# Kernel optimization log

Measured on AMD Instinct MI355X. Metric: run time of the kernel, lower is better.

The kernel has to match this reference:

```python
import jax, jax.numpy as jnp
import numpy as np

K = 20
EPS = 1e-5
NEG_SLOPE = 0.2


def knn(x, k):
    # x: [B, C, N] -> idx [B, N, k] of nearest neighbors (negative sq-dist topk)
    inner = -2.0 * jnp.einsum('bcn,bcm->bnm', x, x)
    xx = jnp.sum(x * x, axis=1)  # [B, N]
    d = -xx[:, :, None] - inner - xx[:, None, :]
    return jax.lax.top_k(d, k)[1]


def get_graph_feature(x, k):
    # x: [B, C, N] -> [B, 2C, N, k]
    idx = knn(x, k)
    xt = jnp.transpose(x, (0, 2, 1))            # [B, N, C]
    feat = jax.vmap(lambda a, i: a[i])(xt, idx)  # [B, N, k, C]
    center = xt[:, :, None, :]
    out = jnp.concatenate([feat - center, jnp.broadcast_to(center, feat.shape)], axis=-1)
    return jnp.transpose(out, (0, 3, 1, 2))


def conv_bn_lrelu(x, w, g, b):
    # 1x1 conv + BatchNorm2d (batch stats, training mode) + LeakyReLU(0.2)
    y = jnp.einsum('oc,bcnk->bonk', w, x)
    mu = jnp.mean(y, axis=(0, 2, 3), keepdims=True)
    var = jnp.mean((y - mu) ** 2, axis=(0, 2, 3), keepdims=True)
    y = (y - mu) * jax.lax.rsqrt(var + EPS)
    y = y * g[None, :, None, None] + b[None, :, None, None]
    return jnp.where(y >= 0, y, NEG_SLOPE * y)


def lrelu(y):
    return jnp.where(y >= 0, y, NEG_SLOPE * y)


def setup_inputs() -> dict:
    key = jax.random.key(0)
    ks = jax.random.split(key, 24)
    B, N = 8, 4096
    d = {}
    d['x'] = jax.random.normal(ks[0], (B, 3, N), dtype=jnp.float32)
    def wconv(k_, o, c):
        return jax.random.normal(k_, (o, c), dtype=jnp.float32) * (1.0 / np.sqrt(c))
    d['w1'] = wconv(ks[1], 32, 6)
    d['g1'] = 1.0 + 0.1 * jax.random.normal(ks[2], (32,), dtype=jnp.float32)
    d['b1'] = 0.1 * jax.random.normal(ks[3], (32,), dtype=jnp.float32)
    d['w2'] = wconv(ks[4], 64, 70)
    d['g2'] = 1.0 + 0.1 * jax.random.normal(ks[5], (64,), dtype=jnp.float32)
    d['b2'] = 0.1 * jax.random.normal(ks[6], (64,), dtype=jnp.float32)
    d['wd1'] = wconv(ks[7], 64, 64)
    d['gd1'] = 1.0 + 0.1 * jax.random.normal(ks[8], (64,), dtype=jnp.float32)
    d['bd1'] = 0.1 * jax.random.normal(ks[9], (64,), dtype=jnp.float32)
    d['wd2'] = wconv(ks[10], 64, 128)
    d['gd2'] = 1.0 + 0.1 * jax.random.normal(ks[11], (64,), dtype=jnp.float32)
    d['bd2'] = 0.1 * jax.random.normal(ks[12], (64,), dtype=jnp.float32)
    d['W2d'] = jax.random.normal(ks[13], (128, 128), dtype=jnp.float32) * (1.0 / np.sqrt(128))
    d['b2d'] = 0.1 * jax.random.normal(ks[14], (128,), dtype=jnp.float32)
    d['W3d'] = jax.random.normal(ks[15], (64, 128), dtype=jnp.float32) * (1.0 / np.sqrt(128))
    d['b3d'] = 0.1 * jax.random.normal(ks[16], (64,), dtype=jnp.float32)
    d['W4d'] = jax.random.normal(ks[17], (11, 64), dtype=jnp.float32) * (1.0 / np.sqrt(64))
    d['b4d'] = 0.1 * jax.random.normal(ks[18], (11,), dtype=jnp.float32)
    return d


def reference(x, w1, g1, b1, w2, g2, b2, wd1, gd1, bd1, wd2, gd2, bd2,
              W2d, b2d, W3d, b3d, W4d, b4d):
    x1_gf = get_graph_feature(x, K)                    # [B, 6, N, k]
    x1_max = jnp.max(conv_bn_lrelu(x1_gf, w1, g1, b1), axis=-1)  # [B, 32, N]
    x2_gf = jnp.concatenate([x1_gf, get_graph_feature(x1_max, K)], axis=1)  # [B, 70, N, k]
    x2_max = jnp.max(conv_bn_lrelu(x2_gf, w2, g2, b2), axis=-1)  # [B, 64, N]
    xd1 = jnp.max(conv_bn_lrelu(get_graph_feature(x1_max, K), wd1, gd1, bd1), axis=-1)  # [B, 64, N]
    xd2 = jnp.max(conv_bn_lrelu(get_graph_feature(x2_max, K), wd2, gd2, bd2), axis=-1)  # [B, 64, N]
    h = jnp.concatenate([xd1, xd2], axis=1)            # [B, 128, N]
    h = h.reshape(1, -1, 128)                          # faithful row-major view
    h = jnp.mean(h, axis=1)                            # [1, 128]
    h = lrelu(h @ W2d.T + b2d)
    h = lrelu(h @ W3d.T + b3d)
    return lrelu(h @ W4d.T + b4d)                      # [1, 11]
```

## Files before the change

### kernel.cpp

```cpp
#include <hip/hip_runtime.h>

#define BB 8
#define NN 4096
#define KK 20
constexpr float EPSV = 1e-5f;
constexpr float SLOPE = 0.2f;

typedef __bf16 bfrag __attribute__((ext_vector_type(8)));
typedef float floatx4 __attribute__((ext_vector_type(4)));
typedef unsigned short us8 __attribute__((ext_vector_type(8)));

__device__ __forceinline__ float lrelu(float v) { return v >= 0.f ? v : SLOPE * v; }

__device__ __forceinline__ unsigned short bf16rn(float f) {
    unsigned int u = __float_as_uint(f);
    return (unsigned short)((u + 0x7FFFu + ((u >> 16) & 1u)) >> 16);
}
__device__ __forceinline__ float bf16up(unsigned short h) {
    return __uint_as_float(((unsigned int)h) << 16);
}

__device__ __forceinline__ void gl2lds16(const void* g, void* l) {
    __builtin_amdgcn_global_load_lds(
        (const __attribute__((address_space(1))) unsigned int*)g,
        (__attribute__((address_space(3))) unsigned int*)l, 16, 0, 0);
}

__global__ void zero_kernel(float* p, int n) {
    int i = blockIdx.x * 256 + threadIdx.x;
    if (i < n) p[i] = 0.f;
}

template<int C>
__global__ void halfnorm_kernel(const float* __restrict__ src, float* __restrict__ hng) {
    int n = blockIdx.x * 256 + threadIdx.x;
    int b = blockIdx.y;
    float s = 0.f;
    #pragma unroll
    for (int c = 0; c < C; c++) { float v = src[(b * C + c) * NN + n]; s += v * v; }
    hng[b * NN + n] = 0.5f * s;
}

template<int C>
__global__ void pack_kernel(const float* __restrict__ src, unsigned short* __restrict__ pk) {
    constexpr int NCH = C / 4;
    int i = blockIdx.x * 256 + threadIdx.x;
    int b = blockIdx.y;
    int n = i / NCH, j = i % NCH;
    us8 v;
    if (j < C / 8) {
        int c0 = j * 8;
        #pragma unroll
        for (int cc = 0; cc < 8; cc++)
            v[cc] = bf16rn(src[(b * C + c0 + cc) * NN + n]);
    } else {
        int c0 = (j - C / 8) * 8;
        #pragma unroll
        for (int cc = 0; cc < 8; cc++) {
            float f = src[(b * C + c0 + cc) * NN + n];
            unsigned short h = bf16rn(f);
            v[cc] = bf16rn(f - bf16up(h));
        }
    }
    int phys = j ^ (n & (NCH - 1));
    *(us8*)(pk + ((size_t)(b * NN + n) * NCH + phys) * 8) = v;
}

__global__ void pack3_kernel(const float* __restrict__ src,
                             unsigned short* __restrict__ pa, unsigned short* __restrict__ pb) {
    int n = blockIdx.x * 256 + threadIdx.x;
    int b = blockIdx.y;
    unsigned short h[3], l[3];
    #pragma unroll
    for (int c = 0; c < 3; c++) {
        float f = src[(b * 3 + c) * NN + n];
        h[c] = bf16rn(f);
        l[c] = bf16rn(f - bf16up(h[c]));
    }
    unsigned short A[32], B[32];
    #pragma unroll
    for (int k = 0; k < 32; k++) { A[k] = 0; B[k] = 0; }
    #pragma unroll
    for (int c = 0; c < 3; c++) {
        A[c] = h[c];     A[3 + c] = l[c];  A[6 + c] = h[c];  A[9 + c] = l[c];
        B[c] = h[c];     B[3 + c] = l[c];  B[6 + c] = l[c];  B[9 + c] = h[c];
    }
    size_t base = (size_t)(b * NN + n) * 32;
    #pragma unroll
    for (int j = 0; j < 4; j++) {
        int phys = j ^ (n & 3);
        us8 va, vb;
        #pragma unroll
        for (int t = 0; t < 8; t++) { va[t] = A[j * 8 + t]; vb[t] = B[j * 8 + t]; }
        *(us8*)(pa + base + phys * 8) = va;
        *(us8*)(pb + base + phys * 8) = vb;
    }
}

template<int C>
__global__ __launch_bounds__(256) void knn_kernel(const unsigned short* __restrict__ pq,
                                                  const unsigned short* __restrict__ pc,
                                                  const float* __restrict__ hng,
                                                  int* __restrict__ idx) {
    constexpr int RS = (C == 3) ? 32 : 2 * C;
    constexpr int NCHR = RS / 8;
    constexpr int SWM = NCHR - 1;
    __shared__ unsigned short qpack[64 * RS];
    __shared__ unsigned short cpack[128 * RS];
    __shared__ float hn[128];
    __shared__ float pv[64 * 33];
    __shared__ unsigned short pidx[64 * 34];
    __shared__ float tau[64];
    __shared__ int   cnt[64];

    const int b = blockIdx.y;
    const int q0 = blockIdx.x * 64;
    const int tid = threadIdx.x;
    const int lane = tid & 63;
    const int wv = tid >> 6;
    const int fl = lane & 15;
    const int fq = lane >> 4;
    const int wr = (wv >> 1) * 32;
    const int wc = (wv & 1) * 64;

    {
        const char* gq = (const char*)(pq + (size_t)(b * NN + q0) * RS);
        constexpr int PQW = (64 * RS * 2 / 1024) / 4;
        #pragma unroll
        for (int t = 0; t < PQW; t++) {
            int seg = wv * PQW + t;
            gl2lds16(gq + seg * 1024 + lane * 16, (char*)qpack + seg * 1024);
        }
    }
    if (tid < 64) { tau[tid] = -3.4e38f; cnt[tid] = 0; }

    float tv[20]; int ti[20];
    #pragma unroll
    for (int k = 0; k < 20; k++) { tv[k] = -3.4e38f; ti[k] = 0; }

    for (int ch = 0; ch < 32; ch++) {
        const int m0 = ch * 128;
        {
            const char* gc = (const char*)(pc + (size_t)(b * NN + m0) * RS);
            constexpr int PCW = (128 * RS * 2 / 1024) / 4;
            #pragma unroll
            for (int t = 0; t < PCW; t++) {
                int seg = wv * PCW + t;
                gl2lds16(gc + seg * 1024 + lane * 16, (char*)cpack + seg * 1024);
            }
        }
        if (tid < 128) hn[tid] = hng[b * NN + m0 + tid];
        __syncthreads();

        floatx4 acc[2][4];
        #pragma unroll
        for (int r2 = 0; r2 < 2; r2++)
            #pragma unroll
            for (int c2 = 0; c2 < 4; c2++)
                acc[r2][c2] = (floatx4)(0.f);

        if constexpr (C == 3) {
            bfrag a[2];
            #pragma unroll
            for (int r2 = 0; r2 < 2; r2++) {
                int row = wr + r2 * 16 + fl;
                a[r2] = *(const bfrag*)(qpack + row * RS + (fq ^ (row & SWM)) * 8);
            }
            #pragma unroll
            for (int c2 = 0; c2 < 4; c2++) {
                int row = wc + c2 * 16 + fl;
                bfrag bm = *(const bfrag*)(cpack + row * RS + (fq ^ (row & SWM)) * 8);
                #pragma unroll
                for (int r2 = 0; r2 < 2; r2++)
                    acc[r2][c2] = __builtin_amdgcn_mfma_f32_16x16x32_bf16(a[r2], bm, acc[r2][c2], 0, 0, 0);
            }
        } else {
            #pragma unroll
            for (int kk = 0; kk < C / 32; kk++) {
                bfrag ah[2], al[2], bh[4], bl[4];
                #pragma unroll
                for (int r2 = 0; r2 < 2; r2++) {
                    int row = wr + r2 * 16 + fl;
                    ah[r2] = *(const bfrag*)(qpack + row * RS + ((kk * 4 + fq) ^ (row & SWM)) * 8);
                    al[r2] = *(const bfrag*)(qpack + row * RS + ((C / 8 + kk * 4 + fq) ^ (row & SWM)) * 8);
                }
                #pragma unroll
                for (int c2 = 0; c2 < 4; c2++) {
                    int row = wc + c2 * 16 + fl;
                    bh[c2] = *(const bfrag*)(cpack + row * RS + ((kk * 4 + fq) ^ (row & SWM)) * 8);
                    bl[c2] = *(const bfrag*)(cpack + row * RS + ((C / 8 + kk * 4 + fq) ^ (row & SWM)) * 8);
                }
                #pragma unroll
                for (int r2 = 0; r2 < 2; r2++)
                    #pragma unroll
                    for (int c2 = 0; c2 < 4; c2++) {
                        acc[r2][c2] = __builtin_amdgcn_mfma_f32_16x16x32_bf16(ah[r2], bh[c2], acc[r2][c2], 0, 0, 0);
                        acc[r2][c2] = __builtin_amdgcn_mfma_f32_16x16x32_bf16(ah[r2], bl[c2], acc[r2][c2], 0, 0, 0);
                        acc[r2][c2] = __builtin_amdgcn_mfma_f32_16x16x32_bf16(al[r2], bh[c2], acc[r2][c2], 0, 0, 0);
                        acc[r2][c2] = __builtin_amdgcn_mfma_f32_16x16x32_bf16(al[r2], bl[c2], acc[r2][c2], 0, 0, 0);
                    }
            }
        }

        auto filter_one = [&](int c2) {
            float hnv = hn[wc + c2 * 16 + fl];
            #pragma unroll
            for (int r2 = 0; r2 < 2; r2++) {
                const float* tp = &tau[wr + r2 * 16 + fq * 4];
                float t0 = tp[0], t1 = tp[1], t2 = tp[2], t3 = tp[3];
                float ta[4] = {t0, t1, t2, t3};
                #pragma unroll
                for (int reg = 0; reg < 4; reg++) {
                    float s = acc[r2][c2][reg] - hnv;
                    if (s > ta[reg]) {
                        int q = wr + r2 * 16 + fq * 4 + reg;
                        int p = atomicAdd(&cnt[q], 1);
                        if (p < 32) {
                            pv[q * 33 + p] = s;
                            pidx[q * 34 + p] = (unsigned short)(m0 + wc + c2 * 16 + fl);
                        }
                    }
                }
            }
        };
        auto drain = [&]() {
            if (lane < 16) {
                int qd = wv * 16 + lane;
                int n = cnt[qd]; if (n > 32) n = 32;
                for (int t = 0; t < n; t++) {
                    float v = pv[qd * 33 + t];
                    if (v > tv[0]) {
                        tv[0] = v; ti[0] = (int)pidx[qd * 34 + t];
                        #pragma unroll
                        for (int j = 0; j < 19; j++) {
                            if (tv[j] > tv[j + 1]) {
                                float a = tv[j]; tv[j] = tv[j + 1]; tv[j + 1] = a;
                                int bi = ti[j]; ti[j] = ti[j + 1]; ti[j + 1] = bi;
                            }
                        }
                    }
                }
                cnt[qd] = 0;
                tau[qd] = tv[0];
            }
        };

        if (ch == 0) {
            #pragma unroll
            for (int ph = 0; ph < 4; ph++) {
                filter_one(ph);
                __syncthreads();
                drain();
                __syncthreads();
            }
        } else {
            #pragma unroll
            for (int c2 = 0; c2 < 4; c2++) filter_one(c2);
            __syncthreads();
            drain();
        }
    }

    if (lane < 16) {
        int q = q0 + wv * 16 + lane;
        #pragma unroll
        for (int k = 0; k < 20; k++)
            idx[(b * NN + q) * KK + k] = ti[k];
    }
}

template<int COUT>
__global__ void precompute_kernel(const float* __restrict__ src, int C,
                                  const float* __restrict__ w, int CIN, int wd_off, int wc_off,
                                  float* __restrict__ G, float* __restrict__ H,
                                  int initG, int initH) {
    constexpr int MY = 256 / COUT;
    extern __shared__ float lds[];
    float* wd = lds;
    float* wc = lds + C * COUT;
    const int b = blockIdx.y;
    const int tid = threadIdx.y * COUT + threadIdx.x;
    for (int i = tid; i < C * COUT; i += 256) {
        int c = i / COUT, o = i % COUT;
        float a  = w[o * CIN + wd_off + c];
        float cc = w[o * CIN + wc_off + c];
        wd[i] = a;
        wc[i] = cc - a;
    }
    __syncthreads();
    const int o = threadIdx.x;
    for (int it = 0; it < COUT / 4; it++) {
        int m = blockIdx.x * 64 + it * MY + threadIdx.y;
        float g = 0.f, h = 0.f;
        for (int c = 0; c < C; c++) {
            float s = src[(b * C + c) * NN + m];
            g += wd[c * COUT + o] * s;
            h += wc[c * COUT + o] * s;
        }
        int gi = (b * NN + m) * COUT + o;
        if (initG) G[gi] = g; else G[gi] += g;
        if (initH) H[gi] = h; else H[gi] += h;
    }
}

template<int COUT, int GROUPS>
__global__ void conv_stats_kernel(const float* __restrict__ G1, const int* __restrict__ idx1,
                                  const float* __restrict__ G2, const int* __restrict__ idx2,
                                  const float* __restrict__ H, float* __restrict__ stats,
                                  float* __restrict__ MaxY, float* __restrict__ MinY) {
    constexpr int NY = 256 / COUT;
    const int b = blockIdx.y;
    const int o = threadIdx.x;
    const int n = blockIdx.x * NY + threadIdx.y;
    const int base = b * NN + n;
    const float h = H[base * COUT + o];
    float s1 = 0.f, s2 = 0.f;
    float gx = -3.4e38f, gn = 3.4e38f;
    #pragma unroll
    for (int k = 0; k < KK; k++) {
        int i1 = idx1[base * KK + k];
        float g = G1[(b * NN + i1) * COUT + o];
        if (GROUPS == 2) {
            int i2 = idx2[base * KK + k];
            g += G2[(b * NN + i2) * COUT + o];
        }
        float y = g + h;
        s1 += y;
        s2 += y * y;
        gx = fmaxf(gx, g);
        gn = fminf(gn, g);
    }
    MaxY[base * COUT + o] = gx + h;
    MinY[base * COUT + o] = gn + h;

    __shared__ float ls[2 * COUT];
    if (threadIdx.y == 0) { ls[o] = 0.f; ls[COUT + o] = 0.f; }
    __syncthreads();
    atomicAdd(&ls[o], s1);
    atomicAdd(&ls[COUT + o], s2);
    __syncthreads();
    if (threadIdx.y == 0) {
        atomicAdd(&stats[o], ls[o]);
        atomicAdd(&stats[64 + o], ls[COUT + o]);
    }
}

__global__ void finalize_kernel(const float* __restrict__ g, const float* __restrict__ bb,
                                float* __restrict__ stats, int cout, float invP) {
    int o = threadIdx.x;
    if (o >= cout) return;
    float mu  = stats[o] * invP;
    float var = stats[64 + o] * invP - mu * mu;
    float sc  = g[o] * rsqrtf(var + EPSV);
    stats[128 + o] = sc;
    stats[192 + o] = bb[o] - mu * sc;
}

__global__ void apply_kernel(const float* __restrict__ MaxY, const float* __restrict__ MinY,
                             const float* __restrict__ stats, float* __restrict__ out, int cout) {
    int e = blockIdx.x * 256 + threadIdx.x;
    int total = BB * cout * NN;
    if (e >= total) return;
    int n = e & (NN - 1);
    int o = (e >> 12) % cout;
    int b = e / (NN * cout);
    float sc = stats[128 + o], sh = stats[192 + o];
    int si = (b * NN + n) * cout + o;
    float v = (sc >= 0.f) ? MaxY[si] : MinY[si];
    out[e] = lrelu(sc * v + sh);
}

__global__ void mean_kernel(const float* __restrict__ xd1, const float* __restrict__ xd2,
                            float* __restrict__ hsum) {
    __shared__ float bins[128];
    const int tid = threadIdx.x;
    if (tid < 128) bins[tid] = 0.f;
    __syncthreads();
    const int half = BB * 64 * NN;
    const int stride = gridDim.x * 256;
    for (int e = blockIdx.x * 256 + tid; e < half; e += stride)
        atomicAdd(&bins[e & 127], xd1[e]);
    for (int e = blockIdx.x * 256 + tid; e < half; e += stride)
        atomicAdd(&bins[e & 127], xd2[e]);
    __syncthreads();
    if (tid < 128) atomicAdd(&hsum[tid], bins[tid]);
}

__global__ void head_kernel(const float* __restrict__ hsum,
                            const float* __restrict__ W2d, const float* __restrict__ b2d,
                            const float* __restrict__ W3d, const float* __restrict__ b3d,
                            const float* __restrict__ W4d, const float* __restrict__ b4d,
                            float* __restrict__ out) {
    __shared__ float h[128], t1[128], t2[64];
    const int t = threadIdx.x;
    h[t] = hsum[t] * (1.f / 32768.f);
    __syncthreads();
    float a = b2d[t];
    for (int j = 0; j < 128; j++) a += W2d[t * 128 + j] * h[j];
    t1[t] = lrelu(a);
    __syncthreads();
    if (t < 64) {
        float a2 = b3d[t];
        for (int j = 0; j < 128; j++) a2 += W3d[t * 128 + j] * t1[j];
        t2[t] = lrelu(a2);
    }
    __syncthreads();
    if (t < 11) {
        float a3 = b4d[t];
        for (int j = 0; j < 64; j++) a3 += W4d[t * 64 + j] * t2[j];
        out[t] = lrelu(a3);
    }
}

extern "C" void kernel_launch(void* const* d_in, const int* in_sizes, int n_in,
                              void* d_out, int out_size, void* d_ws, size_t ws_size,
                              hipStream_t stream) {
    const float* x   = (const float*)d_in[0];
    const float* w1  = (const float*)d_in[1];
    const float* g1  = (const float*)d_in[2];
    const float* b1  = (const float*)d_in[3];
    const float* w2  = (const float*)d_in[4];
    const float* g2  = (const float*)d_in[5];
    const float* b2  = (const float*)d_in[6];
    const float* wd1 = (const float*)d_in[7];
    const float* gd1 = (const float*)d_in[8];
    const float* bd1 = (const float*)d_in[9];
    const float* wd2 = (const float*)d_in[10];
    const float* gd2 = (const float*)d_in[11];
    const float* bd2 = (const float*)d_in[12];
    const float* W2d = (const float*)d_in[13];
    const float* b2d = (const float*)d_in[14];
    const float* W3d = (const float*)d_in[15];
    const float* b3d = (const float*)d_in[16];
    const float* W4d = (const float*)d_in[17];
    const float* b4d = (const float*)d_in[18];
    float* out = (float*)d_out;

    char* ws = (char*)d_ws;
    size_t off = 0;
    auto alloc = [&](size_t bytes) { char* p = ws + off; off += (bytes + 255) & ~size_t(255); return p; };
    int*   idx1  = (int*)  alloc(BB * NN * KK * 4);
    int*   idx2  = (int*)  alloc(BB * NN * KK * 4);
    int*   idx3  = (int*)  alloc(BB * NN * KK * 4);
    float* x1m   = (float*)alloc(BB * 32 * NN * 4);
    float* x2m   = (float*)alloc(BB * 64 * NN * 4);
    float* xd1   = (float*)alloc(BB * 64 * NN * 4);
    float* xd2   = (float*)alloc(BB * 64 * NN * 4);
    float* G1    = (float*)alloc((size_t)BB * NN * 64 * 4);
    float* G2    = (float*)alloc((size_t)BB * NN * 64 * 4);
    float* H     = (float*)alloc((size_t)BB * NN * 64 * 4);
    float* MaxY  = (float*)alloc((size_t)BB * NN * 64 * 4);
    float* MinY  = (float*)alloc((size_t)BB * NN * 64 * 4);
    float* stats = (float*)alloc(256 * 4);
    float* hsum  = (float*)alloc(128 * 4);
    float* hng   = (float*)alloc(BB * NN * 4);
    unsigned short* pa3  = (unsigned short*)alloc((size_t)BB * NN * 32 * 2);
    unsigned short* pb3  = (unsigned short*)alloc((size_t)BB * NN * 32 * 2);
    unsigned short* pk32 = (unsigned short*)alloc((size_t)BB * NN * 64 * 2);
    unsigned short* pk64 = (unsigned short*)alloc((size_t)BB * NN * 128 * 2);

    const float invP = 1.f / (float)(BB * NN * KK);
    const dim3 knn_grid(NN / 64, BB);
    const dim3 hn_grid(NN / 256, BB);

    zero_kernel<<<1, 256, 0, stream>>>(hsum, 128);

    halfnorm_kernel<3><<<hn_grid, 256, 0, stream>>>(x, hng);
    pack3_kernel<<<dim3(NN / 256, BB), 256, 0, stream>>>(x, pa3, pb3);
    knn_kernel<3><<<knn_grid, 256, 0, stream>>>(pa3, pb3, hng, idx1);

    zero_kernel<<<1, 256, 0, stream>>>(stats, 128);
    precompute_kernel<32><<<dim3(NN / 64, BB), dim3(32, 8), 2 * 3 * 32 * 4, stream>>>(
        x, 3, w1, 6, 0, 3, G1, H, 1, 1);
    conv_stats_kernel<32, 1><<<dim3(NN / 8, BB), dim3(32, 8), 0, stream>>>(
        G1, idx1, nullptr, nullptr, H, stats, MaxY, MinY);
    finalize_kernel<<<1, 64, 0, stream>>>(g1, b1, stats, 32, invP);
    apply_kernel<<<(BB * 32 * NN + 255) / 256, 256, 0, stream>>>(MaxY, MinY, stats, x1m, 32);

    halfnorm_kernel<32><<<hn_grid, 256, 0, stream>>>(x1m, hng);
    pack_kernel<32><<<dim3(NN * 8 / 256, BB), 256, 0, stream>>>(x1m, pk32);
    knn_kernel<32><<<knn_grid, 256, 0, stream>>>(pk32, pk32, hng, idx2);

    zero_kernel<<<1, 256, 0, stream>>>(stats, 128);
    precompute_kernel<64><<<dim3(NN / 64, BB), dim3(64, 4), 2 * 3 * 64 * 4, stream>>>(
        x, 3, w2, 70, 0, 3, G1, H, 1, 1);
    precompute_kernel<64><<<dim3(NN / 64, BB), dim3(64, 4), 2 * 32 * 64 * 4, stream>>>(
        x1m, 32, w2, 70, 6, 38, G2, H, 1, 0);
    conv_stats_kernel<64, 2><<<dim3(NN / 4, BB), dim3(64, 4), 0, stream>>>(
        G1, idx1, G2, idx2, H, stats, MaxY, MinY);
    finalize_kernel<<<1, 64, 0, stream>>>(g2, b2, stats, 64, invP);
    apply_kernel<<<(BB * 64 * NN + 255) / 256, 256, 0, stream>>>(MaxY, MinY, stats, x2m, 64);

    zero_kernel<<<1, 256, 0, stream>>>(stats, 128);
    precompute_kernel<64><<<dim3(NN / 64, BB), dim3(64, 4), 2 * 32 * 64 * 4, stream>>>(
        x1m, 32, wd1, 64, 0, 32, G1, H, 1, 1);
    conv_stats_kernel<64, 1><<<dim3(NN / 4, BB), dim3(64, 4), 0, stream>>>(
        G1, idx2, nullptr, nullptr, H, stats, MaxY, MinY);
    finalize_kernel<<<1, 64, 0, stream>>>(gd1, bd1, stats, 64, invP);
    apply_kernel<<<(BB * 64 * NN + 255) / 256, 256, 0, stream>>>(MaxY, MinY, stats, xd1, 64);

    halfnorm_kernel<64><<<hn_grid, 256, 0, stream>>>(x2m, hng);
    pack_kernel<64><<<dim3(NN * 16 / 256, BB), 256, 0, stream>>>(x2m, pk64);
    knn_kernel<64><<<knn_grid, 256, 0, stream>>>(pk64, pk64, hng, idx3);

    zero_kernel<<<1, 256, 0, stream>>>(stats, 128);
    precompute_kernel<64><<<dim3(NN / 64, BB), dim3(64, 4), 2 * 64 * 64 * 4, stream>>>(
        x2m, 64, wd2, 128, 0, 64, G1, H, 1, 1);
    conv_stats_kernel<64, 1><<<dim3(NN / 4, BB), dim3(64, 4), 0, stream>>>(
        G1, idx3, nullptr, nullptr, H, stats, MaxY, MinY);
    finalize_kernel<<<1, 64, 0, stream>>>(gd2, bd2, stats, 64, invP);
    apply_kernel<<<(BB * 64 * NN + 255) / 256, 256, 0, stream>>>(MaxY, MinY, stats, xd2, 64);

    mean_kernel<<<1024, 256, 0, stream>>>(xd1, xd2, hsum);
    head_kernel<<<1, 128, 0, stream>>>(hsum, W2d, b2d, W3d, b3d, W4d, b4d, out);
}
```

Measured before the change: 1.791 ms.

## Split kNN into seed threshold, parallel candidate filter, and wave top-k select

Replaces the single-pass kNN, which kept a running top-20 over all 4096 candidates, with three kernels. A seed pass computes each query's k-th best score over the first 1024 candidates. A filter pass splits the candidate range over four times more blocks and appends every score above that threshold to a per-query global buffer of 192 slots. A wave-level select pass then extracts the top 20. This is meant to remove the serial per-query insertion and drain overhead and to raise parallelism, at the cost of extra launches, global atomics and scratch traffic, plus a risk of silently dropping candidates when more than 192 pass the threshold.

```diff
diff --git a/kernel.cpp b/kernel.cpp
--- a/kernel.cpp
+++ b/kernel.cpp
@@ -3,6 +3,7 @@
 #define BB 8
 #define NN 4096
 #define KK 20
+#define CAP 192
 constexpr float EPSV = 1e-5f;
 constexpr float SLOPE = 0.2f;
 
@@ -32,13 +33,15 @@
 }
 
 template<int C>
-__global__ void halfnorm_kernel(const float* __restrict__ src, float* __restrict__ hng) {
+__global__ void halfnorm_kernel(const float* __restrict__ src, float* __restrict__ hng,
+                                int* __restrict__ gcnt) {
     int n = blockIdx.x * 256 + threadIdx.x;
     int b = blockIdx.y;
     float s = 0.f;
     #pragma unroll
     for (int c = 0; c < C; c++) { float v = src[(b * C + c) * NN + n]; s += v * v; }
     hng[b * NN + n] = 0.5f * s;
+    gcnt[b * NN + n] = 0;
 }
 
 template<int C>
@@ -98,10 +101,10 @@
 }
 
 template<int C>
-__global__ __launch_bounds__(256) void knn_kernel(const unsigned short* __restrict__ pq,
-                                                  const unsigned short* __restrict__ pc,
-                                                  const float* __restrict__ hng,
-                                                  int* __restrict__ idx) {
+__global__ __launch_bounds__(256) void knn_seed(const unsigned short* __restrict__ pq,
+                                                const unsigned short* __restrict__ pc,
+                                                const float* __restrict__ hng,
+                                                float* __restrict__ taug) {
     constexpr int RS = (C == 3) ? 32 : 2 * C;
     constexpr int NCHR = RS / 8;
     constexpr int SWM = NCHR - 1;
@@ -138,7 +141,7 @@
     #pragma unroll
     for (int k = 0; k < 20; k++) { tv[k] = -3.4e38f; ti[k] = 0; }
 
-    for (int ch = 0; ch < 32; ch++) {
+    for (int ch = 0; ch < 8; ch++) {
         const int m0 = ch * 128;
         {
             const char* gc = (const char*)(pc + (size_t)(b * NN + m0) * RS);
@@ -207,8 +210,7 @@
             #pragma unroll
             for (int r2 = 0; r2 < 2; r2++) {
                 const float* tp = &tau[wr + r2 * 16 + fq * 4];
-                float t0 = tp[0], t1 = tp[1], t2 = tp[2], t3 = tp[3];
-                float ta[4] = {t0, t1, t2, t3};
+                float ta[4] = {tp[0], tp[1], tp[2], tp[3]};
                 #pragma unroll
                 for (int reg = 0; reg < 4; reg++) {
                     float s = acc[r2][c2][reg] - hnv;
@@ -263,9 +265,184 @@
 
     if (lane < 16) {
         int q = q0 + wv * 16 + lane;
-        #pragma unroll
-        for (int k = 0; k < 20; k++)
-            idx[(b * NN + q) * KK + k] = ti[k];
+        taug[b * NN + q] = tv[0];
+    }
+}
+
+template<int C>
+__global__ __launch_bounds__(256) void knn_filter(const unsigned short* __restrict__ pq,
+                                                  const unsigned short* __restrict__ pc,
+                                                  const float* __restrict__ hng,
+                                                  const float* __restrict__ taug,
+                                                  int* __restrict__ gcnt,
+                                                  float* __restrict__ ps,
+                                                  unsigned short* __restrict__ pi) {
+    constexpr int RS = (C == 3) ? 32 : 2 * C;
+    constexpr int NCHR = RS / 8;
+    constexpr int SWM = NCHR - 1;
+    __shared__ unsigned short qpack[64 * RS];
+    __shared__ unsigned short cpack[128 * RS];
+    __shared__ float hn[128];
+    __shared__ float taus[64];
+
+    const int b = blockIdx.z;
+    const int q0 = blockIdx.x * 64;
+    const int mbase = blockIdx.y * 1024;
+    const int tid = threadIdx.x;
+    const int lane = tid & 63;
+    const int wv = tid >> 6;
+    const int fl = lane & 15;
+    const int fq = lane >> 4;
+    const int wr = (wv >> 1) * 32;
+    const int wc = (wv & 1) * 64;
+
+    {
+        const char* gq = (const char*)(pq + (size_t)(b * NN + q0) * RS);
+        constexpr int PQW = (64 * RS * 2 / 1024) / 4;
+        #pragma unroll
+        for (int t = 0; t < PQW; t++) {
+            int seg = wv * PQW + t;
+            gl2lds16(gq + seg * 1024 + lane * 16, (char*)qpack + seg * 1024);
+        }
+    }
+    if (tid < 64) {
+        float t = taug[b * NN + q0 + tid];
+        taus[tid] = t - (1e-6f + 1e-6f * fabsf(t));
+    }
+    __syncthreads();
+
+    float taur[2][4];
+    #pragma unroll
+    for (int r2 = 0; r2 < 2; r2++)
+        #pragma unroll
+        for (int reg = 0; reg < 4; reg++)
+            taur[r2][reg] = taus[wr + r2 * 16 + fq * 4 + reg];
+
+    for (int ch = 0; ch < 8; ch++) {
+        const int m0 = mbase + ch * 128;
+        {
+            const char* gc = (const char*)(pc + (size_t)(b * NN + m0) * RS);
+            constexpr int PCW = (128 * RS * 2 / 1024) / 4;
+            #pragma unroll
+            for (int t = 0; t < PCW; t++) {
+                int seg = wv * PCW + t;
+                gl2lds16(gc + seg * 1024 + lane * 16, (char*)cpack + seg * 1024);
+            }
+        }
+        if (tid < 128) hn[tid] = hng[b * NN + m0 + tid];
+        __syncthreads();
+
+        floatx4 acc[2][4];
+        #pragma unroll
+        for (int r2 = 0; r2 < 2; r2++)
+            #pragma unroll
+            for (int c2 = 0; c2 < 4; c2++)
+                acc[r2][c2] = (floatx4)(0.f);
+
+        if constexpr (C == 3) {
+            bfrag a[2];
+            #pragma unroll
+            for (int r2 = 0; r2 < 2; r2++) {
+                int row = wr + r2 * 16 + fl;
+                a[r2] = *(const bfrag*)(qpack + row * RS + (fq ^ (row & SWM)) * 8);
+            }
+            #pragma unroll
+            for (int c2 = 0; c2 < 4; c2++) {
+                int row = wc + c2 * 16 + fl;
+                bfrag bm = *(const bfrag*)(cpack + row * RS + (fq ^ (row & SWM)) * 8);
+                #pragma unroll
+                for (int r2 = 0; r2 < 2; r2++)
+                    acc[r2][c2] = __builtin_amdgcn_mfma_f32_16x16x32_bf16(a[r2], bm, acc[r2][c2], 0, 0, 0);
+            }
+        } else {
+            #pragma unroll
+            for (int kk = 0; kk < C / 32; kk++) {
+                bfrag ah[2], al[2], bh[4], bl[4];
+                #pragma unroll
+                for (int r2 = 0; r2 < 2; r2++) {
+                    int row = wr + r2 * 16 + fl;
+                    ah[r2] = *(const bfrag*)(qpack + row * RS + ((kk * 4 + fq) ^ (row & SWM)) * 8);
+                    al[r2] = *(const bfrag*)(qpack + row * RS + ((C / 8 + kk * 4 + fq) ^ (row & SWM)) * 8);
+                }
+                #pragma unroll
+                for (int c2 = 0; c2 < 4; c2++) {
+                    int row = wc + c2 * 16 + fl;
+                    bh[c2] = *(const bfrag*)(cpack + row * RS + ((kk * 4 + fq) ^ (row & SWM)) * 8);
+                    bl[c2] = *(const bfrag*)(cpack + row * RS + ((C / 8 + kk * 4 + fq) ^ (row & SWM)) * 8);
+                }
+                #pragma unroll
+                for (int r2 = 0; r2 < 2; r2++)
+                    #pragma unroll
+                    for (int c2 = 0; c2 < 4; c2++) {
+                        acc[r2][c2] = __builtin_amdgcn_mfma_f32_16x16x32_bf16(ah[r2], bh[c2], acc[r2][c2], 0, 0, 0);
+                        acc[r2][c2] = __builtin_amdgcn_mfma_f32_16x16x32_bf16(ah[r2], bl[c2], acc[r2][c2], 0, 0, 0);
+                        acc[r2][c2] = __builtin_amdgcn_mfma_f32_16x16x32_bf16(al[r2], bh[c2], acc[r2][c2], 0, 0, 0);
+                        acc[r2][c2] = __builtin_amdgcn_mfma_f32_16x16x32_bf16(al[r2], bl[c2], acc[r2][c2], 0, 0, 0);
+                    }
+            }
+        }
+
+        #pragma unroll
+        for (int c2 = 0; c2 < 4; c2++) {
+            float hnv = hn[wc + c2 * 16 + fl];
+            #pragma unroll
+            for (int r2 = 0; r2 < 2; r2++) {
+                #pragma unroll
+                for (int reg = 0; reg < 4; reg++) {
+                    float s = acc[r2][c2][reg] - hnv;
+                    if (s > taur[r2][reg]) {
+                        int gq = b * NN + q0 + wr + r2 * 16 + fq * 4 + reg;
+                        int p = atomicAdd(&gcnt[gq], 1);
+                        if (p < CAP) {
+                            ps[(size_t)gq * CAP + p] = s;
+                            pi[(size_t)gq * CAP + p] = (unsigned short)(m0 + wc + c2 * 16 + fl);
+                        }
+                    }
+                }
+            }
+        }
+        __syncthreads();
+    }
+}
+
+__global__ __launch_bounds__(256) void knn_select(const int* __restrict__ gcnt,
+                                                  const float* __restrict__ ps,
+                                                  const unsigned short* __restrict__ pi,
+                                                  int* __restrict__ idx) {
+    const int lane = threadIdx.x & 63;
+    const int wv = threadIdx.x >> 6;
+    const int gq = blockIdx.x * 4 + wv;
+    int n = gcnt[gq]; if (n > CAP) n = CAP;
+
+    float v[3]; int id[3];
+    #pragma unroll
+    for (int r = 0; r < 3; r++) {
+        int e = lane + 64 * r;
+        if (e < n) {
+            v[r] = ps[(size_t)gq * CAP + e];
+            id[r] = (int)pi[(size_t)gq * CAP + e];
+        } else {
+            v[r] = -3.4e38f;
+            id[r] = -1 - e;
+        }
+    }
+
+    #pragma unroll
+    for (int k = 0; k < KK; k++) {
+        float bv = v[0]; int bi = id[0];
+        #pragma unroll
+        for (int r = 1; r < 3; r++)
+            if (v[r] > bv || (v[r] == bv && id[r] < bi)) { bv = v[r]; bi = id[r]; }
+        #pragma unroll
+        for (int off = 32; off > 0; off >>= 1) {
+            float ov = __shfl_xor(bv, off);
+            int oi = __shfl_xor(bi, off);
+            if (ov > bv || (ov == bv && oi < bi)) { bv = ov; bi = oi; }
+        }
+        if (lane == 0) idx[gq * KK + k] = bi;
+        #pragma unroll
+        for (int r = 0; r < 3; r++)
+            if (id[r] == bi) v[r] = -3.4e38f;
     }
 }
 
@@ -454,20 +631,29 @@
     float* stats = (float*)alloc(256 * 4);
     float* hsum  = (float*)alloc(128 * 4);
     float* hng   = (float*)alloc(BB * NN * 4);
+    float* taug  = (float*)alloc(BB * NN * 4);
+    int*   gcnt  = (int*)  alloc(BB * NN * 4);
     unsigned short* pa3  = (unsigned short*)alloc((size_t)BB * NN * 32 * 2);
     unsigned short* pb3  = (unsigned short*)alloc((size_t)BB * NN * 32 * 2);
     unsigned short* pk32 = (unsigned short*)alloc((size_t)BB * NN * 64 * 2);
     unsigned short* pk64 = (unsigned short*)alloc((size_t)BB * NN * 128 * 2);
 
+    float* pscore = G1;
+    unsigned short* pidxg = (unsigned short*)MaxY;
+
     const float invP = 1.f / (float)(BB * NN * KK);
     const dim3 knn_grid(NN / 64, BB);
+    const dim3 filt_grid(NN / 64, 4, BB);
     const dim3 hn_grid(NN / 256, BB);
+    const int  sel_grid = BB * NN / 4;
 
     zero_kernel<<<1, 256, 0, stream>>>(hsum, 128);
 
-    halfnorm_kernel<3><<<hn_grid, 256, 0, stream>>>(x, hng);
+    halfnorm_kernel<3><<<hn_grid, 256, 0, stream>>>(x, hng, gcnt);
     pack3_kernel<<<dim3(NN / 256, BB), 256, 0, stream>>>(x, pa3, pb3);
-    knn_kernel<3><<<knn_grid, 256, 0, stream>>>(pa3, pb3, hng, idx1);
+    knn_seed<3><<<knn_grid, 256, 0, stream>>>(pa3, pb3, hng, taug);
+    knn_filter<3><<<filt_grid, 256, 0, stream>>>(pa3, pb3, hng, taug, gcnt, pscore, pidxg);
+    knn_select<<<sel_grid, 256, 0, stream>>>(gcnt, pscore, pidxg, idx1);
 
     zero_kernel<<<1, 256, 0, stream>>>(stats, 128);
     precompute_kernel<32><<<dim3(NN / 64, BB), dim3(32, 8), 2 * 3 * 32 * 4, stream>>>(
@@ -477,9 +663,11 @@
     finalize_kernel<<<1, 64, 0, stream>>>(g1, b1, stats, 32, invP);
     apply_kernel<<<(BB * 32 * NN + 255) / 256, 256, 0, stream>>>(MaxY, MinY, stats, x1m, 32);
 
-    halfnorm_kernel<32><<<hn_grid, 256, 0, stream>>>(x1m, hng);
+    halfnorm_kernel<32><<<hn_grid, 256, 0, stream>>>(x1m, hng, gcnt);
     pack_kernel<32><<<dim3(NN * 8 / 256, BB), 256, 0, stream>>>(x1m, pk32);
-    knn_kernel<32><<<knn_grid, 256, 0, stream>>>(pk32, pk32, hng, idx2);
+    knn_seed<32><<<knn_grid, 256, 0, stream>>>(pk32, pk32, hng, taug);
+    knn_filter<32><<<filt_grid, 256, 0, stream>>>(pk32, pk32, hng, taug, gcnt, pscore, pidxg);
+    knn_select<<<sel_grid, 256, 0, stream>>>(gcnt, pscore, pidxg, idx2);
 
     zero_kernel<<<1, 256, 0, stream>>>(stats, 128);
     precompute_kernel<64><<<dim3(NN / 64, BB), dim3(64, 4), 2 * 3 * 64 * 4, stream>>>(
@@ -499,9 +687,11 @@
     finalize_kernel<<<1, 64, 0, stream>>>(gd1, bd1, stats, 64, invP);
     apply_kernel<<<(BB * 64 * NN + 255) / 256, 256, 0, stream>>>(MaxY, MinY, stats, xd1, 64);
 
-    halfnorm_kernel<64><<<hn_grid, 256, 0, stream>>>(x2m, hng);
+    halfnorm_kernel<64><<<hn_grid, 256, 0, stream>>>(x2m, hng, gcnt);
     pack_kernel<64><<<dim3(NN * 16 / 256, BB), 256, 0, stream>>>(x2m, pk64);
-    knn_kernel<64><<<knn_grid, 256, 0, stream>>>(pk64, pk64, hng, idx3);
+    knn_seed<64><<<knn_grid, 256, 0, stream>>>(pk64, pk64, hng, taug);
+    knn_filter<64><<<filt_grid, 256, 0, stream>>>(pk64, pk64, hng, taug, gcnt, pscore, pidxg);
+    knn_select<<<sel_grid, 256, 0, stream>>>(gcnt, pscore, pidxg, idx3);
 
     zero_kernel<<<1, 256, 0, stream>>>(stats, 128);
     precompute_kernel<64><<<dim3(NN / 64, BB), dim3(64, 4), 2 * 64 * 64 * 4, stream>>>(
```

Result: slower. 2.211 ms (+23.5%).
